# Optimization experiments

Measured on AMD Instinct MI355X. Metric: run time of the kernel, lower is better.

Reference implementation:

```python
import jax, jax.numpy as jnp
import numpy as np

N_NODES = 50000
N_EDGES = 1600000
IN_FEATS = 512
N_HIDDEN = 128
N_CLASSES = 40


def setup_inputs() -> dict:
    key = jax.random.key(0)
    k1, k2, k3, k4, k5, k6, k7 = jax.random.split(key, 7)
    features = jax.random.normal(k1, (N_NODES, IN_FEATS), dtype=jnp.float32)
    src = jax.random.randint(k2, (N_EDGES,), 0, N_NODES)
    dst = jax.random.randint(k3, (N_EDGES,), 0, N_NODES)
    # Glorot-ish init for weights, zeros for biases (DGL GraphConv defaults)
    W1 = jax.random.normal(k4, (IN_FEATS, N_HIDDEN), dtype=jnp.float32) / np.sqrt(IN_FEATS)
    b1 = jnp.zeros((N_HIDDEN,), dtype=jnp.float32)
    W2 = jax.random.normal(k5, (N_HIDDEN, N_CLASSES), dtype=jnp.float32) / np.sqrt(N_HIDDEN)
    b2 = jnp.zeros((N_CLASSES,), dtype=jnp.float32)
    return {"features": features, "W1": W1, "b1": b1, "W2": W2, "b2": b2,
            "src": src, "dst": dst}


def _norms(src, dst, n_nodes):
    ones = jnp.ones(src.shape[0], dtype=jnp.float32)
    deg_out = jax.ops.segment_sum(ones, src, num_segments=n_nodes)
    deg_in = jax.ops.segment_sum(ones, dst, num_segments=n_nodes)
    # clamp degree >= 1 as DGL does
    norm_src = jax.lax.rsqrt(jnp.maximum(deg_out, 1.0))
    norm_dst = jax.lax.rsqrt(jnp.maximum(deg_in, 1.0))
    return norm_src, norm_dst


def _graph_conv(x, W, b, src, dst, norm_src, norm_dst, n_nodes):
    # DGL GraphConv with norm='both'; in_feats > out_feats so W applied first
    h = x @ W                                   # [N, out]
    h = h * norm_src[:, None]                   # src-side D^{-1/2}
    msgs = h[src]                               # gather [E, out]
    agg = jax.ops.segment_sum(msgs, dst, num_segments=n_nodes)  # scatter-add
    agg = agg * norm_dst[:, None]               # dst-side D^{-1/2}
    return agg + b


def reference(features, W1, b1, W2, b2, src, dst):
    norm_src, norm_dst = _norms(src, dst, N_NODES)
    h = _graph_conv(features, W1, b1, src, dst, norm_src, norm_dst, N_NODES)
    h = jax.nn.relu(h)
    # dropout is identity at inference
    h = _graph_conv(h, W2, b2, src, dst, norm_src, norm_dst, N_NODES)
    return h
```

## Files before the change

kernel.cpp:

```cpp
#include <hip/hip_runtime.h>
#include <hip/hip_bf16.h>

#define N_NODES 50000
#define N_EDGES 1600000
#define IN_FEATS 512
#define N_HIDDEN 128
#define N_CLASSES 40
#define NBKT 782
#define NBLK 800
#define EPB 2000
#define NROWPAD 50048

typedef __attribute__((ext_vector_type(8))) short bf16x8;
typedef __attribute__((ext_vector_type(4))) float f32x4;

__device__ __forceinline__ unsigned short f2bf(float f) {
    unsigned u = __float_as_uint(f);
    u = (u + 0x7FFFu + ((u >> 16) & 1u)) >> 16;
    return (unsigned short)u;
}
__device__ __forceinline__ float bf2f(unsigned short h) {
    return __uint_as_float(((unsigned)h) << 16);
}
__device__ __forceinline__ unsigned pk_bf(float a, float b) {
    __hip_bfloat162 h = __float22bfloat162_rn(make_float2(a, b));
    union { __hip_bfloat162 v; unsigned u; } c;
    c.v = h;
    return c.u;
}

__device__ __forceinline__ void cvt8(float4 a, float4 b, bf16x8& h, bf16x8& l) {
    unsigned h0 = pk_bf(a.x, a.y), h1 = pk_bf(a.z, a.w);
    unsigned h2 = pk_bf(b.x, b.y), h3 = pk_bf(b.z, b.w);
    unsigned l0 = pk_bf(a.x - __uint_as_float(h0 << 16),
                        a.y - __uint_as_float(h0 & 0xffff0000u));
    unsigned l1 = pk_bf(a.z - __uint_as_float(h1 << 16),
                        a.w - __uint_as_float(h1 & 0xffff0000u));
    unsigned l2 = pk_bf(b.x - __uint_as_float(h2 << 16),
                        b.y - __uint_as_float(h2 & 0xffff0000u));
    unsigned l3 = pk_bf(b.z - __uint_as_float(h3 << 16),
                        b.w - __uint_as_float(h3 & 0xffff0000u));
    union U { unsigned u[4]; bf16x8 v; };
    U H; H.u[0] = h0; H.u[1] = h1; H.u[2] = h2; H.u[3] = h3; h = H.v;
    U L; L.u[0] = l0; L.u[1] = l1; L.u[2] = l2; L.u[3] = l3; l = L.v;
}

__device__ __forceinline__ int imin(int a, int b) { return a < b ? a : b; }

__global__ __launch_bounds__(256) void setup_cvt(
    const float* __restrict__ W1, const float* __restrict__ W2,
    unsigned short* __restrict__ W1ch, unsigned short* __restrict__ W1cl,
    unsigned short* __restrict__ W2th, unsigned short* __restrict__ W2tl) {
    int i = blockIdx.x * 256 + threadIdx.x;
    if (i < IN_FEATS * N_HIDDEN) {
        int k = i >> 7, c = i & 127;
        float v = W1[i];
        unsigned short h = f2bf(v);
        int o = (k >> 5) * 4096 + c * 32 + (k & 31);
        W1ch[o] = h;
        W1cl[o] = f2bf(v - bf2f(h));
    } else {
        int j = i - IN_FEATS * N_HIDDEN;
        int n = j >> 7, k = j & 127;
        float v = (n < N_CLASSES) ? W2[k * N_CLASSES + n] : 0.f;
        unsigned short h = f2bf(v);
        W2th[n * 128 + k] = h;
        W2tl[n * 128 + k] = f2bf(v - bf2f(h));
    }
}


#define MFJ(AH, AL, BH, BL, ACC)                                              \
    ACC = __builtin_amdgcn_mfma_f32_16x16x32_bf16(AH, BH, ACC, 0, 0, 0);      \
    ACC = __builtin_amdgcn_mfma_f32_16x16x32_bf16(AH, BL, ACC, 0, 0, 0);      \
    ACC = __builtin_amdgcn_mfma_f32_16x16x32_bf16(AL, BH, ACC, 0, 0, 0);

__global__ __launch_bounds__(256) void megaA(
    const int* __restrict__ src, const int* __restrict__ dst,
    int* __restrict__ histD, int* __restrict__ histS,
    const float* __restrict__ X, const unsigned short* __restrict__ Wch,
    const unsigned short* __restrict__ Wcl, unsigned short* __restrict__ Hb) {
    __shared__ __align__(16) unsigned char smem[16384];
    const int tid = threadIdx.x;

    if (blockIdx.x >= NBKT) {
        int* hd = (int*)smem;
        int* hs = hd + NBKT;
        int b = blockIdx.x - NBKT;
        for (int i = tid; i < NBKT; i += 256) { hd[i] = 0; hs[i] = 0; }
        __syncthreads();
        int e0 = b * EPB;
        for (int i = tid; i < EPB; i += 256) {
            atomicAdd(&hd[dst[e0 + i] >> 6], 1);
            atomicAdd(&hs[src[e0 + i] >> 6], 1);
        }
        __syncthreads();
        for (int i = tid; i < NBKT; i += 256) {
            histD[b * NBKT + i] = hd[i];
            histS[b * NBKT + i] = hs[i];
        }
        return;
    }
    typedef unsigned short ush;
    ush* lds = (ush*)smem;

    const int lane = tid & 63;
    const int wv = tid >> 6;
    const int m = lane & 15;
    const int q = lane >> 4;
    const int q8 = q * 8;
    const int row0 = blockIdx.x * 64;

    const unsigned short* wbh = Wch + (wv * 32 + m) * 32 + q8;
    const unsigned short* wbl = Wcl + (wv * 32 + m) * 32 + q8;

    const int srow = (tid >> 6) * 16 + (tid & 15);
    const int sq8  = ((tid >> 4) & 3) * 8;
    const float* xp = &X[(size_t)imin(row0 + srow, N_NODES - 1) * IN_FEATS + sq8];

    f32x4 acc[4][2];
#pragma unroll
    for (int i = 0; i < 4; i++)
#pragma unroll
        for (int j = 0; j < 2; j++) acc[i][j] = (f32x4){0.f, 0.f, 0.f, 0.f};

    {
        float4 p0 = *(const float4*)(xp);
        float4 p1 = *(const float4*)(xp + 4);
        bf16x8 h, l;
        cvt8(p0, p1, h, l);
        *(bf16x8*)(lds + tid * 8) = h;
        *(bf16x8*)(lds + 2048 + tid * 8) = l;
    }
    float4 a0 = *(const float4*)(xp + 32), a1 = *(const float4*)(xp + 36);
    float4 b0 = *(const float4*)(xp + 64), b1 = *(const float4*)(xp + 68);
    float4 n0 = a0, n1 = a1;
    bf16x8 cbh0 = *(const bf16x8*)(wbh);
    bf16x8 cbh1 = *(const bf16x8*)(wbh + 512);
    bf16x8 cbl0 = *(const bf16x8*)(wbl);
    bf16x8 cbl1 = *(const bf16x8*)(wbl + 512);
    __syncthreads();

    for (int kc = 0; kc < 16; kc++) {
        bf16x8 nbh0 = cbh0, nbh1 = cbh1, nbl0 = cbl0, nbl1 = cbl1;
        if (kc < 15) {
            nbh0 = *(const bf16x8*)(wbh + (kc + 1) * 4096);
            nbh1 = *(const bf16x8*)(wbh + (kc + 1) * 4096 + 512);
            nbl0 = *(const bf16x8*)(wbl + (kc + 1) * 4096);
            nbl1 = *(const bf16x8*)(wbl + (kc + 1) * 4096 + 512);
        }
        if (kc < 13) {
            n0 = *(const float4*)(xp + (kc + 3) * 32);
            n1 = *(const float4*)(xp + (kc + 3) * 32 + 4);
        }
        if (kc < 15) {
            ush* bufw = lds + ((kc + 1) & 1) * 4096;
            bf16x8 h, l;
            cvt8(a0, a1, h, l);
            *(bf16x8*)(bufw + tid * 8) = h;
            *(bf16x8*)(bufw + 2048 + tid * 8) = l;
        }
        const ush* bufr = lds + (kc & 1) * 4096;
        bf16x8 ah0 = *(const bf16x8*)(bufr + (0 * 64 + lane) * 8);
        bf16x8 ah1 = *(const bf16x8*)(bufr + (1 * 64 + lane) * 8);
        bf16x8 ah2 = *(const bf16x8*)(bufr + (2 * 64 + lane) * 8);
        bf16x8 ah3 = *(const bf16x8*)(bufr + (3 * 64 + lane) * 8);
        bf16x8 al0 = *(const bf16x8*)(bufr + 2048 + (0 * 64 + lane) * 8);
        bf16x8 al1 = *(const bf16x8*)(bufr + 2048 + (1 * 64 + lane) * 8);
        bf16x8 al2 = *(const bf16x8*)(bufr + 2048 + (2 * 64 + lane) * 8);
        bf16x8 al3 = *(const bf16x8*)(bufr + 2048 + (3 * 64 + lane) * 8);

        MFJ(ah0, al0, cbh0, cbl0, acc[0][0]) MFJ(ah0, al0, cbh1, cbl1, acc[0][1])
        MFJ(ah1, al1, cbh0, cbl0, acc[1][0]) MFJ(ah1, al1, cbh1, cbl1, acc[1][1])
        MFJ(ah2, al2, cbh0, cbl0, acc[2][0]) MFJ(ah2, al2, cbh1, cbl1, acc[2][1])
        MFJ(ah3, al3, cbh0, cbl0, acc[3][0]) MFJ(ah3, al3, cbh1, cbl1, acc[3][1])

        if (kc < 15) __syncthreads();
        a0 = b0; a1 = b1; b0 = n0; b1 = n1;
        cbh0 = nbh0; cbh1 = nbh1; cbl0 = nbl0; cbl1 = nbl1;
    }

#pragma unroll
    for (int i = 0; i < 4; i++) {
#pragma unroll
        for (int r = 0; r < 4; r++) {
            int grow = row0 + i * 16 + q * 4 + r;
            if (grow < N_NODES) {
#pragma unroll
                for (int j = 0; j < 2; j++)
                    Hb[(size_t)grow * N_HIDDEN + wv * 32 + j * 16 + m] = f2bf(acc[i][j][r]);
            }
        }
    }
}

__global__ __launch_bounds__(256) void p2_local(
    const int* __restrict__ histD, const int* __restrict__ histS,
    int* __restrict__ baseD, int* __restrict__ baseS,
    int* __restrict__ totD, int* __restrict__ totS) {
    int wv = threadIdx.x >> 6, lane = threadIdx.x & 63;
    int w = blockIdx.x * 4 + wv;
    if (w >= NBKT) return;
    int runD = 0, runS = 0;
#pragma unroll
    for (int c = 0; c < 13; c++) {
        int blk = c * 64 + lane;
        int vD = 0, vS = 0;
        if (blk < NBLK) {
            vD = histD[blk * NBKT + w];
            vS = histS[blk * NBKT + w];
        }
        int iD = vD, iS = vS;
#pragma unroll
        for (int off = 1; off < 64; off <<= 1) {
            int tD = __shfl_up(iD, off);
            int tS = __shfl_up(iS, off);
            if (lane >= off) { iD += tD; iS += tS; }
        }
        if (blk < NBLK) {
            baseD[blk * NBKT + w] = runD + iD - vD;
            baseS[blk * NBKT + w] = runS + iS - vS;
        }
        runD += __shfl(iD, 63);
        runS += __shfl(iS, 63);
    }
    if (lane == 0) { totD[w] = runD; totS[w] = runS; }
}

__global__ __launch_bounds__(1024) void p2_small(
    const int* __restrict__ totD, const int* __restrict__ totS,
    int* __restrict__ bucket_base, int* __restrict__ srcb_base,
    int* __restrict__ offsets) {
    __shared__ int part[1024];
    int t = threadIdx.x;
    int v = (t < NBKT) ? totD[t] : 0;
    part[t] = v;
    __syncthreads();
    for (int off = 1; off < 1024; off <<= 1) {
        int x = (t >= off) ? part[t - off] : 0;
        __syncthreads();
        part[t] += x;
        __syncthreads();
    }
    if (t < NBKT) bucket_base[t] = part[t] - v;
    if (t == 0) { bucket_base[NBKT] = N_EDGES; offsets[N_NODES] = N_EDGES; }
    __syncthreads();
    v = (t < NBKT) ? totS[t] : 0;
    part[t] = v;
    __syncthreads();
    for (int off = 1; off < 1024; off <<= 1) {
        int x = (t >= off) ? part[t - off] : 0;
        __syncthreads();
        part[t] += x;
        __syncthreads();
    }
    if (t < NBKT) srcb_base[t] = part[t] - v;
    if (t == 0) srcb_base[NBKT] = N_EDGES;
}

__global__ __launch_bounds__(256) void p3_scatter(
    const int* __restrict__ src, const int* __restrict__ dst,
    const int* __restrict__ baseD, const int* __restrict__ baseS,
    const int* __restrict__ bucket_base, const int* __restrict__ srcb_base,
    unsigned int* __restrict__ edata, unsigned char* __restrict__ srcv) {
    __shared__ int curD[NBKT], curS[NBKT];
    int t = threadIdx.x, b = blockIdx.x;
    for (int i = t; i < NBKT; i += 256) {
        curD[i] = bucket_base[i] + baseD[b * NBKT + i];
        curS[i] = srcb_base[i] + baseS[b * NBKT + i];
    }
    __syncthreads();
    int e0 = b * EPB;
    for (int i = t; i < EPB; i += 256) {
        int s = src[e0 + i], d = dst[e0 + i];
        int slotD = atomicAdd(&curD[d >> 6], 1);
        edata[slotD] = (unsigned)s | ((unsigned)(d & 63) << 16);
        int slotS = atomicAdd(&curS[s >> 6], 1);
        srcv[slotS] = (unsigned char)(s & 63);
    }
}

__global__ __launch_bounds__(256) void p4_fused(
    const int* __restrict__ srcb_base, const unsigned char* __restrict__ srcv,
    const int* __restrict__ bucket_base, const unsigned int* __restrict__ edata,
    int* __restrict__ offsets, float* __restrict__ norm_src,
    float* __restrict__ norm_dst, int* __restrict__ sorted_src) {
    __shared__ int cntS[64], cntD[64], cur[64];
    int t = threadIdx.x, b = blockIdx.x;
    if (t < 64) { cntS[t] = 0; cntD[t] = 0; }
    __syncthreads();
    int s0 = srcb_base[b], s1 = srcb_base[b + 1];
    for (int i = s0 + t; i < s1; i += 256) atomicAdd(&cntS[srcv[i]], 1);
    int d0 = bucket_base[b], d1 = bucket_base[b + 1];
    for (int i = d0 + t; i < d1; i += 256)
        atomicAdd(&cntD[(edata[i] >> 16) & 63], 1);
    __syncthreads();
    if (t == 0) {
        int run = 0;
        for (int i = 0; i < 64; i++) { cur[i] = run; run += cntD[i]; }
    }
    __syncthreads();
    if (t < 64) {
        int node = b * 64 + t;
        if (node < N_NODES) {
            norm_src[node] = rsqrtf(fmaxf((float)cntS[t], 1.0f));
            offsets[node] = d0 + cur[t];
            norm_dst[node] = rsqrtf(fmaxf((float)cntD[t], 1.0f));
        }
    }
    __syncthreads();
    for (int i = d0 + t; i < d1; i += 256) {
        unsigned e = edata[i];
        int slot = atomicAdd(&cur[(e >> 16) & 63], 1);
        sorted_src[d0 + slot] = (int)(e & 0xFFFFu);
    }
}

#define FMA8(W, NS)                                                   \
    acc0 = fmaf(__uint_as_float((W).x << 16), NS, acc0);              \
    acc1 = fmaf(__uint_as_float((W).x & 0xffff0000u), NS, acc1);      \
    acc2 = fmaf(__uint_as_float((W).y << 16), NS, acc2);              \
    acc3 = fmaf(__uint_as_float((W).y & 0xffff0000u), NS, acc3);      \
    acc4 = fmaf(__uint_as_float((W).z << 16), NS, acc4);              \
    acc5 = fmaf(__uint_as_float((W).z & 0xffff0000u), NS, acc5);      \
    acc6 = fmaf(__uint_as_float((W).w << 16), NS, acc6);              \
    acc7 = fmaf(__uint_as_float((W).w & 0xffff0000u), NS, acc7);

__global__ __launch_bounds__(256) void agg1_kernel(
    const int* __restrict__ offsets, const int* __restrict__ sorted_src,
    const unsigned short* __restrict__ Hb, const float* __restrict__ norm_dst,
    const float* __restrict__ norm_src, const float* __restrict__ b1,
    unsigned short* __restrict__ H1h, unsigned short* __restrict__ H1l) {
    int wid = (blockIdx.x * 256 + threadIdx.x) >> 6;
    int lane = threadIdx.x & 63;
    if (wid >= N_NODES) return;
    int start = offsets[wid], end = offsets[wid + 1];
    int quad = lane >> 4;
    int c8 = (lane & 15) * 8;
    float acc0 = 0.f, acc1 = 0.f, acc2 = 0.f, acc3 = 0.f;
    float acc4 = 0.f, acc5 = 0.f, acc6 = 0.f, acc7 = 0.f;
    int base = start;
    for (; base + 16 <= end; base += 16) {
        int e0 = sorted_src[base + quad];
        int e1 = sorted_src[base + 4 + quad];
        int e2 = sorted_src[base + 8 + quad];
        int e3 = sorted_src[base + 12 + quad];
        float n0 = norm_src[e0], n1 = norm_src[e1];
        float n2 = norm_src[e2], n3 = norm_src[e3];
        uint4 w0 = *(const uint4*)&Hb[(size_t)e0 * N_HIDDEN + c8];
        uint4 w1 = *(const uint4*)&Hb[(size_t)e1 * N_HIDDEN + c8];
        uint4 w2 = *(const uint4*)&Hb[(size_t)e2 * N_HIDDEN + c8];
        uint4 w3 = *(const uint4*)&Hb[(size_t)e3 * N_HIDDEN + c8];
        FMA8(w0, n0);
        FMA8(w1, n1);
        FMA8(w2, n2);
        FMA8(w3, n3);
    }
    for (; base + 4 <= end; base += 4) {
        int e = sorted_src[base + quad];
        float n = norm_src[e];
        uint4 w = *(const uint4*)&Hb[(size_t)e * N_HIDDEN + c8];
        FMA8(w, n);
    }
    int rem = end - base;
    if (quad < rem) {
        int e = sorted_src[base + quad];
        float n = norm_src[e];
        uint4 w = *(const uint4*)&Hb[(size_t)e * N_HIDDEN + c8];
        FMA8(w, n);
    }
    acc0 += __shfl_xor(acc0, 16); acc0 += __shfl_xor(acc0, 32);
    acc1 += __shfl_xor(acc1, 16); acc1 += __shfl_xor(acc1, 32);
    acc2 += __shfl_xor(acc2, 16); acc2 += __shfl_xor(acc2, 32);
    acc3 += __shfl_xor(acc3, 16); acc3 += __shfl_xor(acc3, 32);
    acc4 += __shfl_xor(acc4, 16); acc4 += __shfl_xor(acc4, 32);
    acc5 += __shfl_xor(acc5, 16); acc5 += __shfl_xor(acc5, 32);
    acc6 += __shfl_xor(acc6, 16); acc6 += __shfl_xor(acc6, 32);
    acc7 += __shfl_xor(acc7, 16); acc7 += __shfl_xor(acc7, 32);
    if (quad == 0) {
        float nd = norm_dst[wid];
        float ns = norm_src[wid];
        float4 ba = *(const float4*)&b1[c8];
        float4 bb = *(const float4*)&b1[c8 + 4];
        float o[8];
        o[0] = fmaxf(acc0 * nd + ba.x, 0.f) * ns;
        o[1] = fmaxf(acc1 * nd + ba.y, 0.f) * ns;
        o[2] = fmaxf(acc2 * nd + ba.z, 0.f) * ns;
        o[3] = fmaxf(acc3 * nd + ba.w, 0.f) * ns;
        o[4] = fmaxf(acc4 * nd + bb.x, 0.f) * ns;
        o[5] = fmaxf(acc5 * nd + bb.y, 0.f) * ns;
        o[6] = fmaxf(acc6 * nd + bb.z, 0.f) * ns;
        o[7] = fmaxf(acc7 * nd + bb.w, 0.f) * ns;
        unsigned short hh[8], ll[8];
#pragma unroll
        for (int t = 0; t < 8; t++) {
            hh[t] = f2bf(o[t]);
            ll[t] = f2bf(o[t] - bf2f(hh[t]));
        }
        uint4 ph = make_uint4((unsigned)hh[0] | ((unsigned)hh[1] << 16),
                              (unsigned)hh[2] | ((unsigned)hh[3] << 16),
                              (unsigned)hh[4] | ((unsigned)hh[5] << 16),
                              (unsigned)hh[6] | ((unsigned)hh[7] << 16));
        uint4 pl = make_uint4((unsigned)ll[0] | ((unsigned)ll[1] << 16),
                              (unsigned)ll[2] | ((unsigned)ll[3] << 16),
                              (unsigned)ll[4] | ((unsigned)ll[5] << 16),
                              (unsigned)ll[6] | ((unsigned)ll[7] << 16));
        *(uint4*)&H1h[(size_t)wid * N_HIDDEN + c8] = ph;
        *(uint4*)&H1l[(size_t)wid * N_HIDDEN + c8] = pl;
    }
}

__global__ __launch_bounds__(256) void gemm2_kernel(
    const unsigned short* __restrict__ H1h, const unsigned short* __restrict__ H1l,
    const unsigned short* __restrict__ W2th, const unsigned short* __restrict__ W2tl,
    unsigned int* __restrict__ H2u) {
    __shared__ __align__(16) unsigned short Bh[48][136];
    __shared__ __align__(16) unsigned short Bl[48][136];
    const int tid = threadIdx.x;
    for (int i = tid; i < 48 * 16; i += 256) {
        int n = i >> 4, kq = (i & 15) * 8;
        *(uint4*)&Bh[n][kq] = *(const uint4*)&W2th[n * 128 + kq];
        *(uint4*)&Bl[n][kq] = *(const uint4*)&W2tl[n * 128 + kq];
    }
    __syncthreads();
    const int lane = tid & 63;
    const int wave = tid >> 6;
    const int m = lane & 15;
    const int q = lane >> 4;
    const int row0 = blockIdx.x * 128 + wave * 32;

    f32x4 acc[2][3];
#pragma unroll
    for (int i = 0; i < 2; i++)
#pragma unroll
        for (int j = 0; j < 3; j++) acc[i][j] = (f32x4){0.f, 0.f, 0.f, 0.f};

#pragma unroll
    for (int kc = 0; kc < 4; kc++) {
        bf16x8 bh[3], bl[3];
#pragma unroll
        for (int j = 0; j < 3; j++) {
            bh[j] = *(const bf16x8*)&Bh[j * 16 + m][kc * 32 + q * 8];
            bl[j] = *(const bf16x8*)&Bl[j * 16 + m][kc * 32 + q * 8];
        }
#pragma unroll
        for (int i = 0; i < 2; i++) {
            size_t ro = (size_t)(row0 + i * 16 + m) * N_HIDDEN + kc * 32 + q * 8;
            bf16x8 ah = *(const bf16x8*)&H1h[ro];
            bf16x8 al = *(const bf16x8*)&H1l[ro];
#pragma unroll
            for (int j = 0; j < 3; j++) {
                acc[i][j] = __builtin_amdgcn_mfma_f32_16x16x32_bf16(ah, bh[j], acc[i][j], 0, 0, 0);
                acc[i][j] = __builtin_amdgcn_mfma_f32_16x16x32_bf16(ah, bl[j], acc[i][j], 0, 0, 0);
                acc[i][j] = __builtin_amdgcn_mfma_f32_16x16x32_bf16(al, bh[j], acc[i][j], 0, 0, 0);
            }
        }
    }
#pragma unroll
    for (int i = 0; i < 2; i++) {
#pragma unroll
        for (int r = 0; r < 4; r++) {
            int row = row0 + i * 16 + q * 4 + r;
            if (row < N_NODES) {
#pragma unroll
                for (int j = 0; j < 3; j++) {
                    int col = j * 16 + m;
                    if (col < N_CLASSES) {
                        float v = acc[i][j][r];
                        unsigned short h = f2bf(v);
                        unsigned short l = f2bf(v - bf2f(h));
                        H2u[(size_t)row * 48 + col] = ((unsigned)h << 16) | (unsigned)l;
                    }
                }
            }
        }
    }
}

#define ACC4(V)                                                               \
    acc.x += __uint_as_float((V).x & 0xffff0000u) + __uint_as_float((V).x << 16); \
    acc.y += __uint_as_float((V).y & 0xffff0000u) + __uint_as_float((V).y << 16); \
    acc.z += __uint_as_float((V).z & 0xffff0000u) + __uint_as_float((V).z << 16); \
    acc.w += __uint_as_float((V).w & 0xffff0000u) + __uint_as_float((V).w << 16);

__global__ __launch_bounds__(256) void agg2_kernel(
    const int* __restrict__ offsets, const int* __restrict__ sorted_src,
    const unsigned int* __restrict__ H2u, const float* __restrict__ norm_dst,
    const float* __restrict__ b2, float* __restrict__ OUT) {
    int wid = (blockIdx.x * 256 + threadIdx.x) >> 6;
    int lane = threadIdx.x & 63;
    if (wid >= N_NODES) return;
    int start = offsets[wid], end = offsets[wid + 1];
    int quad = lane >> 4;
    int c4 = (lane & 15) * 4;
    bool active = c4 < N_CLASSES;
    float4 acc = make_float4(0.f, 0.f, 0.f, 0.f);
    int base = start;
    for (; base + 16 <= end; base += 16) {
        int e0 = sorted_src[base + quad];
        int e1 = sorted_src[base + 4 + quad];
        int e2 = sorted_src[base + 8 + quad];
        int e3 = sorted_src[base + 12 + quad];
        if (active) {
            uint4 v0 = *(const uint4*)&H2u[(size_t)e0 * 48 + c4];
            uint4 v1 = *(const uint4*)&H2u[(size_t)e1 * 48 + c4];
            uint4 v2 = *(const uint4*)&H2u[(size_t)e2 * 48 + c4];
            uint4 v3 = *(const uint4*)&H2u[(size_t)e3 * 48 + c4];
            ACC4(v0); ACC4(v1); ACC4(v2); ACC4(v3);
        }
    }
    for (; base + 4 <= end; base += 4) {
        int e = sorted_src[base + quad];
        if (active) {
            uint4 v = *(const uint4*)&H2u[(size_t)e * 48 + c4];
            ACC4(v);
        }
    }
    int rem = end - base;
    if (quad < rem && active) {
        int e = sorted_src[base + quad];
        uint4 v = *(const uint4*)&H2u[(size_t)e * 48 + c4];
        ACC4(v);
    }
    acc.x += __shfl_xor(acc.x, 16); acc.x += __shfl_xor(acc.x, 32);
    acc.y += __shfl_xor(acc.y, 16); acc.y += __shfl_xor(acc.y, 32);
    acc.z += __shfl_xor(acc.z, 16); acc.z += __shfl_xor(acc.z, 32);
    acc.w += __shfl_xor(acc.w, 16); acc.w += __shfl_xor(acc.w, 32);
    if (lane < 10) {
        float nd = norm_dst[wid];
        float4 b = *(const float4*)&b2[lane * 4];
        acc.x = acc.x * nd + b.x;
        acc.y = acc.y * nd + b.y;
        acc.z = acc.z * nd + b.z;
        acc.w = acc.w * nd + b.w;
        *(float4*)&OUT[(size_t)wid * N_CLASSES + lane * 4] = acc;
    }
}

extern "C" void kernel_launch(void* const* d_in, const int* in_sizes, int n_in,
                              void* d_out, int out_size, void* d_ws, size_t ws_size,
                              hipStream_t stream) {
    const float* X   = (const float*)d_in[0];
    const float* W1  = (const float*)d_in[1];
    const float* b1  = (const float*)d_in[2];
    const float* W2  = (const float*)d_in[3];
    const float* b2  = (const float*)d_in[4];
    const int*   src = (const int*)d_in[5];
    const int*   dst = (const int*)d_in[6];
    float* out = (float*)d_out;

    float* norm_src   = (float*)d_ws;
    float* norm_dst   = norm_src + N_NODES;
    int*   offsets    = (int*)(norm_dst + N_NODES);
    int*   bucket_base = offsets + N_NODES + 16;
    int*   srcb_base  = bucket_base + 800;
    unsigned int* edata = (unsigned int*)(srcb_base + 800);
    unsigned char* srcv = (unsigned char*)(edata + N_EDGES);
    int*   sorted_src = (int*)(edata + N_EDGES) + 400000;
    int*   regionA    = sorted_src + N_EDGES;
    int*   histD      = regionA;
    int*   histS      = regionA + 625600;
    int*   baseD      = regionA + 1251200;
    int*   baseS      = regionA + 1876800;
    int*   totD       = regionA + 2502400;
    int*   totS       = regionA + 2503200;
    unsigned int* H2u = (unsigned int*)regionA;
    unsigned short* H1h = (unsigned short*)(regionA + 3200000);
    unsigned short* H1l = H1h + (size_t)NROWPAD * N_HIDDEN;
    unsigned short* W1ch = H1l + (size_t)NROWPAD * N_HIDDEN;
    unsigned short* W1cl = W1ch + IN_FEATS * N_HIDDEN;
    unsigned short* W2th = W1cl + IN_FEATS * N_HIDDEN;
    unsigned short* W2tl = W2th + 48 * 128;
    unsigned short* Hb   = W2tl + 48 * 128;

    setup_cvt<<<(IN_FEATS * N_HIDDEN + 48 * 128) / 256, 256, 0, stream>>>(
        W1, W2, W1ch, W1cl, W2th, W2tl);
    megaA<<<NBLK + NBKT, 256, 0, stream>>>(src, dst, histD, histS, X, W1ch, W1cl, Hb);
    p2_local<<<(NBKT + 3) / 4, 256, 0, stream>>>(histD, histS, baseD, baseS, totD, totS);
    p2_small<<<1, 1024, 0, stream>>>(totD, totS, bucket_base, srcb_base, offsets);
    p3_scatter<<<NBLK, 256, 0, stream>>>(src, dst, baseD, baseS, bucket_base, srcb_base,
                                         edata, srcv);
    p4_fused<<<NBKT, 256, 0, stream>>>(srcb_base, srcv, bucket_base, edata,
                                       offsets, norm_src, norm_dst, sorted_src);
    agg1_kernel<<<(N_NODES + 3) / 4, 256, 0, stream>>>(offsets, sorted_src, Hb, norm_dst,
                                                       norm_src, b1, H1h, H1l);
    gemm2_kernel<<<(N_NODES + 127) / 128, 256, 0, stream>>>(H1h, H1l, W2th, W2tl, H2u);
    agg2_kernel<<<(N_NODES + 3) / 4, 256, 0, stream>>>(offsets, sorted_src, H2u, norm_dst, b2, out);
}
```

Before: 361.3 us.

## Restructure layer-1 GEMM so each wave owns 16 rows, dropping LDS staging

The layer-1 projection in megaA stops staging X tiles through double-buffered LDS with block-wide barriers. Each wave now loads its own 16 rows of X straight from global memory, converts them to bf16 hi/lo in registers, and computes all 128 output columns with 8 accumulators, reading all W1 fragments from global or L2 each k-step. It also adds a min-blocks hint of 4 to launch_bounds and shrinks shared memory to just the histogram arrays, aiming to remove barrier stalls and raise occupancy. In exchange, every wave re-reads the whole W1 chunk, which multiplies weight traffic, and there is no prefetch of weight fragments ahead of the MFMAs.

```diff
diff --git a/kernel.cpp b/kernel.cpp
--- a/kernel.cpp
+++ b/kernel.cpp
@@ -75,17 +75,15 @@
     ACC = __builtin_amdgcn_mfma_f32_16x16x32_bf16(AH, BL, ACC, 0, 0, 0);      \
     ACC = __builtin_amdgcn_mfma_f32_16x16x32_bf16(AL, BH, ACC, 0, 0, 0);
 
-__global__ __launch_bounds__(256) void megaA(
+__global__ __launch_bounds__(256, 4) void megaA(
     const int* __restrict__ src, const int* __restrict__ dst,
     int* __restrict__ histD, int* __restrict__ histS,
     const float* __restrict__ X, const unsigned short* __restrict__ Wch,
     const unsigned short* __restrict__ Wcl, unsigned short* __restrict__ Hb) {
-    __shared__ __align__(16) unsigned char smem[16384];
+    __shared__ int hd[NBKT], hs[NBKT];
     const int tid = threadIdx.x;
 
     if (blockIdx.x >= NBKT) {
-        int* hd = (int*)smem;
-        int* hs = hd + NBKT;
         int b = blockIdx.x - NBKT;
         for (int i = tid; i < NBKT; i += 256) { hd[i] = 0; hs[i] = 0; }
         __syncthreads();
@@ -101,9 +99,6 @@
         }
         return;
     }
-    typedef unsigned short ush;
-    ush* lds = (ush*)smem;
-
     const int lane = tid & 63;
     const int wv = tid >> 6;
     const int m = lane & 15;
@@ -111,85 +106,68 @@
     const int q8 = q * 8;
     const int row0 = blockIdx.x * 64;
 
-    const unsigned short* wbh = Wch + (wv * 32 + m) * 32 + q8;
-    const unsigned short* wbl = Wcl + (wv * 32 + m) * 32 + q8;
-
-    const int srow = (tid >> 6) * 16 + (tid & 15);
-    const int sq8  = ((tid >> 4) & 3) * 8;
-    const float* xp = &X[(size_t)imin(row0 + srow, N_NODES - 1) * IN_FEATS + sq8];
-
-    f32x4 acc[4][2];
-#pragma unroll
-    for (int i = 0; i < 4; i++)
-#pragma unroll
-        for (int j = 0; j < 2; j++) acc[i][j] = (f32x4){0.f, 0.f, 0.f, 0.f};
-
-    {
-        float4 p0 = *(const float4*)(xp);
-        float4 p1 = *(const float4*)(xp + 4);
-        bf16x8 h, l;
-        cvt8(p0, p1, h, l);
-        *(bf16x8*)(lds + tid * 8) = h;
-        *(bf16x8*)(lds + 2048 + tid * 8) = l;
-    }
-    float4 a0 = *(const float4*)(xp + 32), a1 = *(const float4*)(xp + 36);
-    float4 b0 = *(const float4*)(xp + 64), b1 = *(const float4*)(xp + 68);
-    float4 n0 = a0, n1 = a1;
-    bf16x8 cbh0 = *(const bf16x8*)(wbh);
-    bf16x8 cbh1 = *(const bf16x8*)(wbh + 512);
-    bf16x8 cbl0 = *(const bf16x8*)(wbl);
-    bf16x8 cbl1 = *(const bf16x8*)(wbl + 512);
-    __syncthreads();
+    const int myrow = imin(row0 + wv * 16 + m, N_NODES - 1);
+    const float* xp = &X[(size_t)myrow * IN_FEATS + q8];
+    const unsigned short* wb = Wch + m * 32 + q8;
+    const unsigned short* wl = Wcl + m * 32 + q8;
+
+    f32x4 acc[8];
+#pragma unroll
+    for (int n = 0; n < 8; n++) acc[n] = (f32x4){0.f, 0.f, 0.f, 0.f};
+
+    float4 cx0 = *(const float4*)(xp),      cx1 = *(const float4*)(xp + 4);
+    float4 px0 = *(const float4*)(xp + 32), px1 = *(const float4*)(xp + 36);
 
     for (int kc = 0; kc < 16; kc++) {
-        bf16x8 nbh0 = cbh0, nbh1 = cbh1, nbl0 = cbl0, nbl1 = cbl1;
-        if (kc < 15) {
-            nbh0 = *(const bf16x8*)(wbh + (kc + 1) * 4096);
-            nbh1 = *(const bf16x8*)(wbh + (kc + 1) * 4096 + 512);
-            nbl0 = *(const bf16x8*)(wbl + (kc + 1) * 4096);
-            nbl1 = *(const bf16x8*)(wbl + (kc + 1) * 4096 + 512);
-        }
-        if (kc < 13) {
-            n0 = *(const float4*)(xp + (kc + 3) * 32);
-            n1 = *(const float4*)(xp + (kc + 3) * 32 + 4);
-        }
-        if (kc < 15) {
-            ush* bufw = lds + ((kc + 1) & 1) * 4096;
-            bf16x8 h, l;
-            cvt8(a0, a1, h, l);
-            *(bf16x8*)(bufw + tid * 8) = h;
-            *(bf16x8*)(bufw + 2048 + tid * 8) = l;
-        }
-        const ush* bufr = lds + (kc & 1) * 4096;
-        bf16x8 ah0 = *(const bf16x8*)(bufr + (0 * 64 + lane) * 8);
-        bf16x8 ah1 = *(const bf16x8*)(bufr + (1 * 64 + lane) * 8);
-        bf16x8 ah2 = *(const bf16x8*)(bufr + (2 * 64 + lane) * 8);
-        bf16x8 ah3 = *(const bf16x8*)(bufr + (3 * 64 + lane) * 8);
-        bf16x8 al0 = *(const bf16x8*)(bufr + 2048 + (0 * 64 + lane) * 8);
-        bf16x8 al1 = *(const bf16x8*)(bufr + 2048 + (1 * 64 + lane) * 8);
-        bf16x8 al2 = *(const bf16x8*)(bufr + 2048 + (2 * 64 + lane) * 8);
-        bf16x8 al3 = *(const bf16x8*)(bufr + 2048 + (3 * 64 + lane) * 8);
-
-        MFJ(ah0, al0, cbh0, cbl0, acc[0][0]) MFJ(ah0, al0, cbh1, cbl1, acc[0][1])
-        MFJ(ah1, al1, cbh0, cbl0, acc[1][0]) MFJ(ah1, al1, cbh1, cbl1, acc[1][1])
-        MFJ(ah2, al2, cbh0, cbl0, acc[2][0]) MFJ(ah2, al2, cbh1, cbl1, acc[2][1])
-        MFJ(ah3, al3, cbh0, cbl0, acc[3][0]) MFJ(ah3, al3, cbh1, cbl1, acc[3][1])
-
-        if (kc < 15) __syncthreads();
-        a0 = b0; a1 = b1; b0 = n0; b1 = n1;
-        cbh0 = nbh0; cbh1 = nbh1; cbl0 = nbl0; cbl1 = nbl1;
-    }
-
-#pragma unroll
-    for (int i = 0; i < 4; i++) {
-#pragma unroll
-        for (int r = 0; r < 4; r++) {
-            int grow = row0 + i * 16 + q * 4 + r;
-            if (grow < N_NODES) {
-#pragma unroll
-                for (int j = 0; j < 2; j++)
-                    Hb[(size_t)grow * N_HIDDEN + wv * 32 + j * 16 + m] = f2bf(acc[i][j][r]);
-            }
+        float4 nx0 = px0, nx1 = px1;
+        if (kc < 14) {
+            nx0 = *(const float4*)(xp + (kc + 2) * 32);
+            nx1 = *(const float4*)(xp + (kc + 2) * 32 + 4);
+        }
+        bf16x8 ah, al;
+        cvt8(cx0, cx1, ah, al);
+        const unsigned short* wbk = wb + kc * 4096;
+        const unsigned short* wlk = wl + kc * 4096;
+        {
+            bf16x8 bh0 = *(const bf16x8*)(wbk);
+            bf16x8 bh1 = *(const bf16x8*)(wbk + 512);
+            bf16x8 bh2 = *(const bf16x8*)(wbk + 1024);
+            bf16x8 bh3 = *(const bf16x8*)(wbk + 1536);
+            bf16x8 bl0 = *(const bf16x8*)(wlk);
+            bf16x8 bl1 = *(const bf16x8*)(wlk + 512);
+            bf16x8 bl2 = *(const bf16x8*)(wlk + 1024);
+            bf16x8 bl3 = *(const bf16x8*)(wlk + 1536);
+            MFJ(ah, al, bh0, bl0, acc[0])
+            MFJ(ah, al, bh1, bl1, acc[1])
+            MFJ(ah, al, bh2, bl2, acc[2])
+            MFJ(ah, al, bh3, bl3, acc[3])
+        }
+        {
+            bf16x8 bh4 = *(const bf16x8*)(wbk + 2048);
+            bf16x8 bh5 = *(const bf16x8*)(wbk + 2560);
+            bf16x8 bh6 = *(const bf16x8*)(wbk + 3072);
+            bf16x8 bh7 = *(const bf16x8*)(wbk + 3584);
+            bf16x8 bl4 = *(const bf16x8*)(wlk + 2048);
+            bf16x8 bl5 = *(const bf16x8*)(wlk + 2560);
+            bf16x8 bl6 = *(const bf16x8*)(wlk + 3072);
+            bf16x8 bl7 = *(const bf16x8*)(wlk + 3584);
+            MFJ(ah, al, bh4, bl4, acc[4])
+            MFJ(ah, al, bh5, bl5, acc[5])
+            MFJ(ah, al, bh6, bl6, acc[6])
+            MFJ(ah, al, bh7, bl7, acc[7])
+        }
+        cx0 = px0; cx1 = px1;
+        px0 = nx0; px1 = nx1;
+    }
+
+    const int orow = row0 + wv * 16 + q * 4;
+#pragma unroll
+    for (int r = 0; r < 4; r++) {
+        int grow = orow + r;
+        if (grow < N_NODES) {
+#pragma unroll
+            for (int n = 0; n < 8; n++)
+                Hb[(size_t)grow * N_HIDDEN + n * 16 + m] = f2bf(acc[n][r]);
         }
     }
 }
```

Result: slower. 388.1 us (+7.4%).

## Process two K-chunks per barrier in megaA; store sorted sources as 16-bit

Applied to the files above, without the earlier changes.

The first-layer GEMM in megaA now converts and stages two 32-wide K chunks per LDS buffer, so it runs 8 iterations with half as many barriers. Shared memory doubles to 32 KB per block. Weight fragments are now loaded directly inside each chunk rather than register-prefetched a step ahead, which may expose load latency. Separately, the destination-sorted source index array is stored as unsigned short, since node ids fit in 16 bits, halving index traffic in both aggregation kernels.

```diff
diff --git a/kernel.cpp b/kernel.cpp
--- a/kernel.cpp
+++ b/kernel.cpp
@@ -75,12 +75,35 @@
     ACC = __builtin_amdgcn_mfma_f32_16x16x32_bf16(AH, BL, ACC, 0, 0, 0);      \
     ACC = __builtin_amdgcn_mfma_f32_16x16x32_bf16(AL, BH, ACC, 0, 0, 0);
 
+#define CHUNK_COMPUTE(FRAGBASE, KC)                                           \
+    {                                                                         \
+        const unsigned short* wk  = wbh + (KC) * 4096;                        \
+        const unsigned short* wkl = wbl + (KC) * 4096;                        \
+        bf16x8 bh0 = *(const bf16x8*)(wk);                                    \
+        bf16x8 bh1 = *(const bf16x8*)(wk + 512);                              \
+        bf16x8 bl0 = *(const bf16x8*)(wkl);                                   \
+        bf16x8 bl1 = *(const bf16x8*)(wkl + 512);                             \
+        const unsigned short* fb = (FRAGBASE);                                \
+        bf16x8 ah0 = *(const bf16x8*)(fb + (0 * 64 + lane) * 8);              \
+        bf16x8 ah1 = *(const bf16x8*)(fb + (1 * 64 + lane) * 8);              \
+        bf16x8 ah2 = *(const bf16x8*)(fb + (2 * 64 + lane) * 8);              \
+        bf16x8 ah3 = *(const bf16x8*)(fb + (3 * 64 + lane) * 8);              \
+        bf16x8 al0 = *(const bf16x8*)(fb + 2048 + (0 * 64 + lane) * 8);       \
+        bf16x8 al1 = *(const bf16x8*)(fb + 2048 + (1 * 64 + lane) * 8);       \
+        bf16x8 al2 = *(const bf16x8*)(fb + 2048 + (2 * 64 + lane) * 8);       \
+        bf16x8 al3 = *(const bf16x8*)(fb + 2048 + (3 * 64 + lane) * 8);       \
+        MFJ(ah0, al0, bh0, bl0, acc[0][0]) MFJ(ah0, al0, bh1, bl1, acc[0][1]) \
+        MFJ(ah1, al1, bh0, bl0, acc[1][0]) MFJ(ah1, al1, bh1, bl1, acc[1][1]) \
+        MFJ(ah2, al2, bh0, bl0, acc[2][0]) MFJ(ah2, al2, bh1, bl1, acc[2][1]) \
+        MFJ(ah3, al3, bh0, bl0, acc[3][0]) MFJ(ah3, al3, bh1, bl1, acc[3][1]) \
+    }
+
 __global__ __launch_bounds__(256) void megaA(
     const int* __restrict__ src, const int* __restrict__ dst,
     int* __restrict__ histD, int* __restrict__ histS,
     const float* __restrict__ X, const unsigned short* __restrict__ Wch,
     const unsigned short* __restrict__ Wcl, unsigned short* __restrict__ Hb) {
-    __shared__ __align__(16) unsigned char smem[16384];
+    __shared__ __align__(16) unsigned char smem[32768];
     const int tid = threadIdx.x;
 
     if (blockIdx.x >= NBKT) {
@@ -125,59 +148,40 @@
         for (int j = 0; j < 2; j++) acc[i][j] = (f32x4){0.f, 0.f, 0.f, 0.f};
 
     {
-        float4 p0 = *(const float4*)(xp);
-        float4 p1 = *(const float4*)(xp + 4);
+        float4 c00 = *(const float4*)(xp),      c01 = *(const float4*)(xp + 4);
+        float4 c10 = *(const float4*)(xp + 32), c11 = *(const float4*)(xp + 36);
         bf16x8 h, l;
-        cvt8(p0, p1, h, l);
+        cvt8(c00, c01, h, l);
         *(bf16x8*)(lds + tid * 8) = h;
         *(bf16x8*)(lds + 2048 + tid * 8) = l;
-    }
-    float4 a0 = *(const float4*)(xp + 32), a1 = *(const float4*)(xp + 36);
-    float4 b0 = *(const float4*)(xp + 64), b1 = *(const float4*)(xp + 68);
-    float4 n0 = a0, n1 = a1;
-    bf16x8 cbh0 = *(const bf16x8*)(wbh);
-    bf16x8 cbh1 = *(const bf16x8*)(wbh + 512);
-    bf16x8 cbl0 = *(const bf16x8*)(wbl);
-    bf16x8 cbl1 = *(const bf16x8*)(wbl + 512);
-    __syncthreads();
-
-    for (int kc = 0; kc < 16; kc++) {
-        bf16x8 nbh0 = cbh0, nbh1 = cbh1, nbl0 = cbl0, nbl1 = cbl1;
-        if (kc < 15) {
-            nbh0 = *(const bf16x8*)(wbh + (kc + 1) * 4096);
-            nbh1 = *(const bf16x8*)(wbh + (kc + 1) * 4096 + 512);
-            nbl0 = *(const bf16x8*)(wbl + (kc + 1) * 4096);
-            nbl1 = *(const bf16x8*)(wbl + (kc + 1) * 4096 + 512);
-        }
-        if (kc < 13) {
-            n0 = *(const float4*)(xp + (kc + 3) * 32);
-            n1 = *(const float4*)(xp + (kc + 3) * 32 + 4);
-        }
-        if (kc < 15) {
-            ush* bufw = lds + ((kc + 1) & 1) * 4096;
+        cvt8(c10, c11, h, l);
+        *(bf16x8*)(lds + 4096 + tid * 8) = h;
+        *(bf16x8*)(lds + 6144 + tid * 8) = l;
+    }
+    float4 a00 = *(const float4*)(xp + 64), a01 = *(const float4*)(xp + 68);
+    float4 a10 = *(const float4*)(xp + 96), a11 = *(const float4*)(xp + 100);
+    __syncthreads();
+
+    for (int pp = 0; pp < 8; pp++) {
+        if (pp < 7) {
+            ush* bs = lds + ((pp + 1) & 1) * 8192;
             bf16x8 h, l;
-            cvt8(a0, a1, h, l);
-            *(bf16x8*)(bufw + tid * 8) = h;
-            *(bf16x8*)(bufw + 2048 + tid * 8) = l;
-        }
-        const ush* bufr = lds + (kc & 1) * 4096;
-        bf16x8 ah0 = *(const bf16x8*)(bufr + (0 * 64 + lane) * 8);
-        bf16x8 ah1 = *(const bf16x8*)(bufr + (1 * 64 + lane) * 8);
-        bf16x8 ah2 = *(const bf16x8*)(bufr + (2 * 64 + lane) * 8);
-        bf16x8 ah3 = *(const bf16x8*)(bufr + (3 * 64 + lane) * 8);
-        bf16x8 al0 = *(const bf16x8*)(bufr + 2048 + (0 * 64 + lane) * 8);
-        bf16x8 al1 = *(const bf16x8*)(bufr + 2048 + (1 * 64 + lane) * 8);
-        bf16x8 al2 = *(const bf16x8*)(bufr + 2048 + (2 * 64 + lane) * 8);
-        bf16x8 al3 = *(const bf16x8*)(bufr + 2048 + (3 * 64 + lane) * 8);
-
-        MFJ(ah0, al0, cbh0, cbl0, acc[0][0]) MFJ(ah0, al0, cbh1, cbl1, acc[0][1])
-        MFJ(ah1, al1, cbh0, cbl0, acc[1][0]) MFJ(ah1, al1, cbh1, cbl1, acc[1][1])
-        MFJ(ah2, al2, cbh0, cbl0, acc[2][0]) MFJ(ah2, al2, cbh1, cbl1, acc[2][1])
-        MFJ(ah3, al3, cbh0, cbl0, acc[3][0]) MFJ(ah3, al3, cbh1, cbl1, acc[3][1])
-
-        if (kc < 15) __syncthreads();
-        a0 = b0; a1 = b1; b0 = n0; b1 = n1;
-        cbh0 = nbh0; cbh1 = nbh1; cbl0 = nbl0; cbl1 = nbl1;
+            cvt8(a00, a01, h, l);
+            *(bf16x8*)(bs + tid * 8) = h;
+            *(bf16x8*)(bs + 2048 + tid * 8) = l;
+            cvt8(a10, a11, h, l);
+            *(bf16x8*)(bs + 4096 + tid * 8) = h;
+            *(bf16x8*)(bs + 6144 + tid * 8) = l;
+        }
+        if (pp < 6) {
+            const float* xq = xp + (pp + 2) * 64;
+            a00 = *(const float4*)(xq);      a01 = *(const float4*)(xq + 4);
+            a10 = *(const float4*)(xq + 32); a11 = *(const float4*)(xq + 36);
+        }
+        const ush* br = lds + (pp & 1) * 8192;
+        CHUNK_COMPUTE(br,        2 * pp)
+        CHUNK_COMPUTE(br + 4096, 2 * pp + 1)
+        if (pp < 7) __syncthreads();
     }
 
 #pragma unroll
@@ -284,7 +288,7 @@
     const int* __restrict__ srcb_base, const unsigned char* __restrict__ srcv,
     const int* __restrict__ bucket_base, const unsigned int* __restrict__ edata,
     int* __restrict__ offsets, float* __restrict__ norm_src,
-    float* __restrict__ norm_dst, int* __restrict__ sorted_src) {
+    float* __restrict__ norm_dst, unsigned short* __restrict__ sorted_src) {
     __shared__ int cntS[64], cntD[64], cur[64];
     int t = threadIdx.x, b = blockIdx.x;
     if (t < 64) { cntS[t] = 0; cntD[t] = 0; }
@@ -312,7 +316,7 @@
     for (int i = d0 + t; i < d1; i += 256) {
         unsigned e = edata[i];
         int slot = atomicAdd(&cur[(e >> 16) & 63], 1);
-        sorted_src[d0 + slot] = (int)(e & 0xFFFFu);
+        sorted_src[d0 + slot] = (unsigned short)(e & 0xFFFFu);
     }
 }
 
@@ -327,7 +331,7 @@
     acc7 = fmaf(__uint_as_float((W).w & 0xffff0000u), NS, acc7);
 
 __global__ __launch_bounds__(256) void agg1_kernel(
-    const int* __restrict__ offsets, const int* __restrict__ sorted_src,
+    const int* __restrict__ offsets, const unsigned short* __restrict__ sorted_src,
     const unsigned short* __restrict__ Hb, const float* __restrict__ norm_dst,
     const float* __restrict__ norm_src, const float* __restrict__ b1,
     unsigned short* __restrict__ H1h, unsigned short* __restrict__ H1l) {
@@ -484,7 +488,7 @@
     acc.w += __uint_as_float((V).w & 0xffff0000u) + __uint_as_float((V).w << 16);
 
 __global__ __launch_bounds__(256) void agg2_kernel(
-    const int* __restrict__ offsets, const int* __restrict__ sorted_src,
+    const int* __restrict__ offsets, const unsigned short* __restrict__ sorted_src,
     const unsigned int* __restrict__ H2u, const float* __restrict__ norm_dst,
     const float* __restrict__ b2, float* __restrict__ OUT) {
     int wid = (blockIdx.x * 256 + threadIdx.x) >> 6;
@@ -556,8 +560,9 @@
     int*   srcb_base  = bucket_base + 800;
     unsigned int* edata = (unsigned int*)(srcb_base + 800);
     unsigned char* srcv = (unsigned char*)(edata + N_EDGES);
-    int*   sorted_src = (int*)(edata + N_EDGES) + 400000;
-    int*   regionA    = sorted_src + N_EDGES;
+    unsigned short* sorted_src =
+        (unsigned short*)((int*)(edata + N_EDGES) + 400000);
+    int*   regionA    = (int*)(edata + N_EDGES) + 400000 + 800000;
     int*   histD      = regionA;
     int*   histS      = regionA + 625600;
     int*   baseD      = regionA + 1251200;
```

New measurement: 357.1 us. About the same (-1.2%).
